# Performance work log

Hardware: AMD Instinct MI355X
Metric: run time of the kernel (lower is better)

## Reference

```python
import jax, jax.numpy as jnp
import numpy as np

IB = 8      # input/hidden activation bits
ABMVM = 8   # gate activation bits after MVM
ABNM = 8    # near-memory compute bits
NL = 0.05   # analog noise level
CY_DIV = 2.0
CY_SCALE = 2.0


def quant_pass(x, wb, sign):
    # Faithful port of QuantFunc.forward: clip/clamp then fake-quant (round to grid).
    if wb is None or wb == 0:
        return x
    if sign:
        delta = 0.0 if wb == 1 else 1.0 / (2.0 ** (wb - 1))
        x = jnp.clip(x, -1.0 + delta, 1.0 - delta)
    else:
        x = jnp.clip(x, 0.0, 1.0)
    if wb == 1:
        return jnp.sign(x)
    scale = 2.0 ** (wb - 1) if sign else 2.0 ** wb
    return jnp.round(x * scale) / scale


def setup_inputs() -> dict:
    key = jax.random.key(0)
    ks = jax.random.split(key, 7)
    B, I, H = 4096, 1024, 1024
    return {
        "input": jax.random.normal(ks[0], (B, I), jnp.float32),
        "hx": jax.random.normal(ks[1], (B, H), jnp.float32),
        "cx": jax.random.normal(ks[2], (B, H), jnp.float32),
        "weight_ih": jax.random.normal(ks[3], (4 * H, I), jnp.float32) * 0.1,
        "weight_hh": jax.random.normal(ks[4], (4 * H, H), jnp.float32) * 0.1,
        "bias_ih": jax.random.normal(ks[5], (4 * H,), jnp.float32) * 0.1,
        "bias_hh": jax.random.normal(ks[6], (4 * H,), jnp.float32) * 0.1,
        "train": 0,
    }


def reference(input, hx, cx, weight_ih, weight_hh, bias_ih, bias_hh, train):
    # Per-call Gaussian noise (simulated analog hardware); fixed key for reproducibility.
    nk = jax.random.split(jax.random.key(42), 4)
    noise_w_ih = jax.random.normal(nk[0], weight_ih.T.shape, weight_ih.dtype) * weight_ih.max() * NL
    noise_w_hh = jax.random.normal(nk[1], weight_hh.T.shape, weight_hh.dtype) * weight_hh.max() * NL
    noise_b_ih = jax.random.normal(nk[2], bias_ih.shape, bias_ih.dtype) * bias_ih.max() * NL
    noise_b_hh = jax.random.normal(nk[3], bias_hh.shape, bias_hh.dtype) * bias_hh.max() * NL

    # gates: [B, 4H]
    gates = (quant_pass(input, IB, True) @ (weight_ih.T + noise_w_ih) + bias_ih + noise_b_ih
             + quant_pass(hx, IB, True) @ (weight_hh.T + noise_w_hh) + bias_hh + noise_b_hh)

    ingate, forgetgate, cellgate, outgate = jnp.split(gates, 4, axis=1)
    ingate = quant_pass(jax.nn.sigmoid(ingate), ABMVM, False)
    forgetgate = quant_pass(jax.nn.sigmoid(forgetgate), ABMVM, False)
    cellgate = quant_pass(jnp.tanh(cellgate), ABMVM, True)
    outgate = quant_pass(jax.nn.sigmoid(outgate), ABMVM, False)

    cy = quant_pass((quant_pass(forgetgate * cx, ABNM, True)
                     + quant_pass(ingate * cellgate, ABNM, True)) / CY_DIV, ABNM, True)
    hy = quant_pass(outgate * quant_pass(jnp.tanh(cy * CY_SCALE), ABNM, True), ABNM, True)
    return (hy, cy)
```

## Files before the change

### kernel.cpp

```cpp
#include <hip/hip_runtime.h>
#include <hip/hip_bf16.h>
#include <stdint.h>
#include <stddef.h>


#define PART 1

typedef __attribute__((ext_vector_type(8))) short bf16x8;
typedef __attribute__((ext_vector_type(4))) float f32x4;

#define BATCH 4096

#define WS_A_OFF    ((size_t)0)
#define WS_B_OFF    ((size_t)16 << 20)
#define WS_BIAS_OFF ((size_t)48 << 20)
#define WS_MAX_OFF  (WS_BIAS_OFF + 16384)

__host__ __device__ inline void tf2x32(uint32_t k0, uint32_t k1,
                                       uint32_t x0, uint32_t x1,
                                       uint32_t &o0, uint32_t &o1)
{
  const uint32_t k2 = k0 ^ k1 ^ 0x1BD11BDAu;
#define TFR(r) { x0 += x1; x1 = (x1 << (r)) | (x1 >> (32 - (r))); x1 ^= x0; }
  x0 += k0; x1 += k1;
  TFR(13) TFR(15) TFR(26) TFR(6)
  x0 += k1; x1 += k2 + 1u;
  TFR(17) TFR(29) TFR(16) TFR(24)
  x0 += k2; x1 += k0 + 2u;
  TFR(13) TFR(15) TFR(26) TFR(6)
  x0 += k0; x1 += k1 + 3u;
  TFR(17) TFR(29) TFR(16) TFR(24)
  x0 += k1; x1 += k2 + 4u;
  TFR(13) TFR(15) TFR(26) TFR(6)
  x0 += k2; x1 += k0 + 5u;
#undef TFR
  o0 = x0; o1 = x1;
}

__device__ inline uint32_t jax_bits32(uint32_t k0, uint32_t k1, uint32_t i, uint32_t size)
{
#if PART
  uint32_t a, b;
  tf2x32(k0, k1, 0u, i, a, b);
  return a ^ b;
#else
  uint32_t half = size >> 1, a, b;
  if (i < half) { tf2x32(k0, k1, i, i + half, a, b); return a; }
  tf2x32(k0, k1, i - half, i, a, b); return b;
#endif
}

__device__ inline float bits_to_normal(uint32_t bits)
{
  float f = __uint_as_float((bits >> 9) | 0x3F800000u) - 1.0f;
  const float lo = -0x1.fffffep-1f;
  float u = fmaxf(lo, f * 2.0f + lo);
  float w = -log1pf(-u * u);
  float p;
  if (w < 5.0f) {
    w -= 2.5f;
    p = 2.81022636e-08f;
    p = fmaf(p, w, 3.43273939e-07f);
    p = fmaf(p, w, -3.5233877e-06f);
    p = fmaf(p, w, -4.39150654e-06f);
    p = fmaf(p, w, 0.00021858087f);
    p = fmaf(p, w, -0.00125372503f);
    p = fmaf(p, w, -0.00417768164f);
    p = fmaf(p, w, 0.246640727f);
    p = fmaf(p, w, 1.50140941f);
  } else {
    w = sqrtf(w) - 3.0f;
    p = -0.000200214257f;
    p = fmaf(p, w, 0.000100950558f);
    p = fmaf(p, w, 0.00134934322f);
    p = fmaf(p, w, -0.00367342844f);
    p = fmaf(p, w, 0.00573950773f);
    p = fmaf(p, w, -0.0076224613f);
    p = fmaf(p, w, 0.00943887047f);
    p = fmaf(p, w, 1.00167406f);
    p = fmaf(p, w, 2.83297682f);
  }
  return 0x1.6a09e6p+0f * (p * u);
}

__device__ inline float quantS8(float x)
{
  x = fminf(fmaxf(x, -0.9921875f), 0.9921875f);
  return rintf(x * 128.0f) * 0.0078125f;
}
__device__ inline float quantU8(float x)
{
  x = fminf(fmaxf(x, 0.0f), 1.0f);
  return rintf(x * 256.0f) * 0.00390625f;
}

#define LOG2E 1.44269504088896340736f
__device__ inline float sigmoid_fast(float x)
{
  float e = __builtin_amdgcn_exp2f(x * -LOG2E);
  return __builtin_amdgcn_rcpf(1.0f + e);
}
__device__ inline float tanh_fast(float x)
{
  float a = fabsf(x);
  float e = __builtin_amdgcn_exp2f(a * (-2.0f * LOG2E));
  float t = (1.0f - e) * __builtin_amdgcn_rcpf(1.0f + e);
  return copysignf(t, x);
}

__device__ inline unsigned short f2bf(float x)
{
  uint32_t b = __float_as_uint(x);
  return (unsigned short)((b + 0x7FFFu + ((b >> 16) & 1u)) >> 16);
}
__device__ inline float bf2f(unsigned short u) { return __uint_as_float(((uint32_t)u) << 16); }

__device__ inline float dec_max(uint32_t u)
{
  uint32_t bits = (u & 0x80000000u) ? (u ^ 0x80000000u) : ~u;
  return __uint_as_float(bits);
}

__global__ void init_max(uint32_t* mx)
{
  if (threadIdx.x < 4) mx[threadIdx.x] = 0u;
}

__global__ void kmax_all(const float4* __restrict__ wih, const float4* __restrict__ whh,
                         const float4* __restrict__ bih, const float4* __restrict__ bhh,
                         uint32_t* __restrict__ mx)
{
  const int blk = blockIdx.x;
  const float4* src; int n4, bl, nb; uint32_t* out;
  if (blk < 1024)      { src = wih; n4 = 1048576; bl = blk;        nb = 1024; out = mx + 0; }
  else if (blk < 2048) { src = whh; n4 = 1048576; bl = blk - 1024; nb = 1024; out = mx + 1; }
  else if (blk < 2052) { src = bih; n4 = 1024;    bl = blk - 2048; nb = 4;    out = mx + 2; }
  else                 { src = bhh; n4 = 1024;    bl = blk - 2052; nb = 4;    out = mx + 3; }

  float m = -3.4e38f;
  for (int i = bl * 256 + threadIdx.x; i < n4; i += nb * 256) {
    float4 v = src[i];
    m = fmaxf(fmaxf(m, fmaxf(v.x, v.y)), fmaxf(v.z, v.w));
  }
  for (int off = 32; off; off >>= 1) m = fmaxf(m, __shfl_down(m, off, 64));
  __shared__ float sm[4];
  if ((threadIdx.x & 63) == 0) sm[threadIdx.x >> 6] = m;
  __syncthreads();
  if (threadIdx.x == 0) {
    float bm = fmaxf(fmaxf(sm[0], sm[1]), fmaxf(sm[2], sm[3]));
    uint32_t bits = __float_as_uint(bm);
    uint32_t enc = (bits & 0x80000000u) ? ~bits : (bits | 0x80000000u);
    atomicMax(out, enc);
  }
}

__global__ void build_all(const float* __restrict__ wih, const float* __restrict__ whh,
                          const float4* __restrict__ in, const float4* __restrict__ hxp,
                          const float* __restrict__ bih, const float* __restrict__ bhh,
                          unsigned short* __restrict__ A, unsigned short* __restrict__ B,
                          float* __restrict__ biasE, const uint32_t* __restrict__ mxenc,
                          uint32_t kih0, uint32_t kih1, uint32_t khh0, uint32_t khh1,
                          uint32_t kbi0, uint32_t kbi1, uint32_t kbh0, uint32_t kbh1)
{
  const uint32_t blk = blockIdx.x;
  if (blk < 16384u) {
    uint32_t t = blk * 256u + threadIdx.x;
    uint32_t arr = t >> 21;
    uint32_t r = t & 2097151u;
    uint32_t kp = r & 511u;
    uint32_t n = r >> 9;
    const float* w = arr ? whh : wih;
    float mx = dec_max(mxenc[arr]);
    uint32_t key0 = arr ? khh0 : kih0, key1 = arr ? khh1 : kih1;
    uint32_t k0 = kp * 2u;
    uint32_t hiw = 0u, low = 0u;
#pragma unroll
    for (int e = 0; e < 2; ++e) {
      uint32_t k = k0 + (uint32_t)e;
      float nrm = bits_to_normal(jax_bits32(key0, key1, k * 4096u + n, 4194304u));
      float weff = w[(size_t)n * 1024u + k] + (nrm * mx) * 0.05f;
      unsigned short hi = f2bf(weff);
      unsigned short lob = f2bf(weff - bf2f(hi));
      hiw |= ((uint32_t)hi) << (16 * e);
      low |= ((uint32_t)lob) << (16 * e);
    }
    uint32_t np = (n & 1023u) * 4u + (n >> 10);
    size_t base = (size_t)np * 4096u + (arr ? 1024u : 0u) + k0;
    *reinterpret_cast<uint32_t*>(B + base) = hiw;
    *reinterpret_cast<uint32_t*>(B + base + 2048u) = low;
  } else if (blk < 24576u) {
    int t = (int)(blk - 16384u) * 256 + threadIdx.x;
    int b = t >> 9;
    int kq = t & 511;
    float4 v = (kq < 256) ? in[b * 256 + kq] : hxp[b * 256 + (kq - 256)];
    unsigned short o[4];
    o[0] = f2bf(quantS8(v.x)); o[1] = f2bf(quantS8(v.y));
    o[2] = f2bf(quantS8(v.z)); o[3] = f2bf(quantS8(v.w));
    *reinterpret_cast<uint64_t*>(A + (size_t)t * 4) = *reinterpret_cast<uint64_t*>(o);
  } else {
    uint32_t j = (blk - 24576u) * 256u + threadIdx.x;
    float mi = dec_max(mxenc[2]), mh = dec_max(mxenc[3]);
    float ni = (bits_to_normal(jax_bits32(kbi0, kbi1, j, 4096u)) * mi) * 0.05f;
    float nh = (bits_to_normal(jax_bits32(kbh0, kbh1, j, 4096u)) * mh) * 0.05f;
    biasE[(j & 1023u) * 4u + (j >> 10)] = ((bih[j] + ni) + bhh[j]) + nh;
  }
}

__device__ __forceinline__ void gload_lds16(const void* g, void* l)
{
  __builtin_amdgcn_global_load_lds((__attribute__((address_space(1))) void*)g,
                                   (__attribute__((address_space(3))) void*)l, 16, 0, 0);
}

#define VM0  asm volatile("s_waitcnt vmcnt(0)" ::: "memory")
#define NOVM
#define SBAR __builtin_amdgcn_s_barrier()
#define SCB  __builtin_amdgcn_sched_barrier(0)

#define BUFSZ 32768

#define STAGE_A(ts_, bi_)                                                         \
    { unsigned char* la_ = lds + (bi_) * BUFSZ; const int ka_ = (ts_) * 32;       \
      gload_lds16(Ar0 + ka_, la_ + tid * 16);                                     \
      gload_lds16(Ar1 + ka_, la_ + 4096 + tid * 16);                              \
      gload_lds16(Ar2 + ka_, la_ + 8192 + tid * 16);                              \
      gload_lds16(Ar3 + ka_, la_ + 12288 + tid * 16); }
#define STAGE_BH(ts_, bi_)                                                        \
    { unsigned char* la_ = lds + (bi_) * BUFSZ; const int ka_ = (ts_) * 32;       \
      gload_lds16(Br0 + ka_, la_ + 16384 + tid * 16);                             \
      gload_lds16(Br1 + ka_, la_ + 16384 + 4096 + tid * 16); }
#define STAGE_BL(ts_, bi_)                                                        \
    { unsigned char* la_ = lds + (bi_) * BUFSZ; const int ka_ = (ts_) * 32;       \
      gload_lds16(Br0 + 2048 + ka_, la_ + 24576 + tid * 16);                      \
      gload_lds16(Br1 + 2048 + ka_, la_ + 24576 + 4096 + tid * 16); }

#define TILE_ONE(t_, BUF_, BUFN_, DO_STAGE_, VM_ASM_)                             \
  {                                                                               \
    const unsigned char* pa_  = lds + (BUF_) * BUFSZ + aoff;                      \
    const unsigned char* pbh_ = lds + (BUF_) * BUFSZ + 16384 + boffU;             \
    const unsigned char* pbl_ = lds + (BUF_) * BUFSZ + 24576 + boffU;             \
    bf16x8 bh_[4], bl_[4], afL_[4], afH_[4];                                      \
    _Pragma("unroll") for (int n_ = 0; n_ < 4; ++n_)                              \
      bh_[n_] = *(const bf16x8*)(pbh_ + n_ * 1024);                               \
    _Pragma("unroll") for (int m_ = 0; m_ < 4; ++m_)                              \
      afL_[m_] = *(const bf16x8*)(pa_ + m_ * 1024);                               \
    if (DO_STAGE_) { STAGE_A((t_) + 1, BUFN_); }                                  \
    __builtin_amdgcn_s_setprio(1);                                                \
    _Pragma("unroll") for (int m_ = 0; m_ < 4; ++m_)                              \
      _Pragma("unroll") for (int n_ = 0; n_ < 4; ++n_)                            \
        acc[m_][n_] = __builtin_amdgcn_mfma_f32_16x16x32_bf16(afL_[m_], bh_[n_],  \
                                                              acc[m_][n_], 0, 0, 0); \
    __builtin_amdgcn_s_setprio(0);                                                \
    _Pragma("unroll") for (int m_ = 0; m_ < 4; ++m_)                              \
      afH_[m_] = *(const bf16x8*)(pa_ + (4 + m_) * 1024);                         \
    if (DO_STAGE_) { STAGE_BH((t_) + 1, BUFN_); }                                 \
    __builtin_amdgcn_s_setprio(1);                                                \
    _Pragma("unroll") for (int m_ = 0; m_ < 4; ++m_)                              \
      _Pragma("unroll") for (int n_ = 0; n_ < 4; ++n_)                            \
        acc[4 + m_][n_] = __builtin_amdgcn_mfma_f32_16x16x32_bf16(afH_[m_], bh_[n_], \
                                                              acc[4 + m_][n_], 0, 0, 0); \
    __builtin_amdgcn_s_setprio(0);                                                \
    _Pragma("unroll") for (int n_ = 0; n_ < 4; ++n_)                              \
      bl_[n_] = *(const bf16x8*)(pbl_ + n_ * 1024);                               \
    if (DO_STAGE_) { STAGE_BL((t_) + 1, BUFN_); }                                 \
    __builtin_amdgcn_s_setprio(1);                                                \
    _Pragma("unroll") for (int m_ = 0; m_ < 4; ++m_)                              \
      _Pragma("unroll") for (int n_ = 0; n_ < 4; ++n_)                            \
        acc[m_][n_] = __builtin_amdgcn_mfma_f32_16x16x32_bf16(afL_[m_], bl_[n_],  \
                                                              acc[m_][n_], 0, 0, 0); \
    _Pragma("unroll") for (int m_ = 0; m_ < 4; ++m_)                              \
      _Pragma("unroll") for (int n_ = 0; n_ < 4; ++n_)                            \
        acc[4 + m_][n_] = __builtin_amdgcn_mfma_f32_16x16x32_bf16(afH_[m_], bl_[n_], \
                                                              acc[4 + m_][n_], 0, 0, 0); \
    __builtin_amdgcn_s_setprio(0);                                                \
    VM_ASM_;                                                                      \
    SBAR; SCB;                                                                    \
  }

#define LTS 136

__global__ __launch_bounds__(256, 2) void gemm_gates(
    const unsigned short* __restrict__ A,
    const unsigned short* __restrict__ B,
    const float* __restrict__ bias,
    const float* __restrict__ cx,
    float* __restrict__ hy,
    float* __restrict__ cy)
{
  extern __shared__ unsigned char lds[];
  const int tid  = threadIdx.x;
  const int lane = tid & 63;
  const int wave = tid >> 6;
  const int wr = wave >> 1;
  const int wc = wave & 1;

  const int bid = blockIdx.x;
  const int wg  = (bid & 7) * 64 + (bid >> 3);
  const int brow = (wg & 15) * 256;
  const int bcol = (wg >> 4) * 128;

#define CHUNK_SRC(c_, sr_, sk_) \
    { int p_ = (c_) >> 3, lc_ = ((c_) & 7) ^ (p_ & 7); \
      sr_ = p_ * 2 + (lc_ >> 2); sk_ = (lc_ & 3) * 8; }
  int sr, sk;
  CHUNK_SRC(tid,        sr, sk);
  const unsigned short* Ar0 = A + (size_t)(brow + sr) * 2048 + sk;
  const unsigned short* Br0 = B + (size_t)(bcol + sr) * 4096 + sk;
  CHUNK_SRC(tid + 256,  sr, sk);
  const unsigned short* Ar1 = A + (size_t)(brow + sr) * 2048 + sk;
  const unsigned short* Br1 = B + (size_t)(bcol + sr) * 4096 + sk;
  CHUNK_SRC(tid + 512,  sr, sk);
  const unsigned short* Ar2 = A + (size_t)(brow + sr) * 2048 + sk;
  CHUNK_SRC(tid + 768,  sr, sk);
  const unsigned short* Ar3 = A + (size_t)(brow + sr) * 2048 + sk;
#undef CHUNK_SRC

  const int lrh = (lane & 15) >> 1;
  const int chk = ((((lane & 1) << 2) | (lane >> 4)) ^ lrh);
  const int aoff  = wr * 8192 + lrh * 128 + chk * 16;
  const int boffU = wc * 4096 + lrh * 128 + chk * 16;

  f32x4 acc[8][4] = {};

  STAGE_A(0, 0); STAGE_BH(0, 0); STAGE_BL(0, 0);
  VM0;
  SBAR; SCB;

#pragma unroll 1
  for (int t = 0; t < 63; ++t) {
    TILE_ONE(t, (t & 1), ((t + 1) & 1), 1, VM0);
  }
  TILE_ONE(63, 1, 0, 0, NOVM);

  float* LT = (float*)lds;
  const int col_local0 = wc * 64 + (lane & 15);
  const int lrow = (lane >> 4) << 2;
  const int h = tid & 31;
  const int hg = (bcol >> 2) + h;

#pragma unroll
  for (int hh = 0; hh < 2; ++hh) {
    __syncthreads();
#pragma unroll
    for (int m = 0; m < 4; ++m) {
#pragma unroll
      for (int n = 0; n < 4; ++n) {
        const int cl = col_local0 + n * 16;
        const float bv = bias[bcol + cl];
        const int lr0 = wr * 64 + m * 16 + lrow;
#pragma unroll
        for (int r = 0; r < 4; ++r)
          LT[(lr0 + r) * LTS + cl] = acc[hh * 4 + m][n][r] + bv;
      }
    }
    __syncthreads();
#pragma unroll
    for (int i = 0; i < 16; ++i) {
      const int lr = (tid >> 5) * 16 + i;
      const int grow = brow + ((lr >> 6) << 7) + hh * 64 + (lr & 63);
      const float4 q = *(const float4*)(LT + lr * LTS + 4 * h);
      const size_t oidx = (size_t)grow * 1024 + hg;
      float ing = quantU8(sigmoid_fast(q.x));
      float fg  = quantU8(sigmoid_fast(q.y));
      float cg  = quantS8(tanh_fast(q.z));
      float og  = quantU8(sigmoid_fast(q.w));
      float c0  = cx[oidx];
      float cyv = quantS8((quantS8(fg * c0) + quantS8(ing * cg)) * 0.5f);
      float hyv = quantS8(og * quantS8(tanh_fast(cyv * 2.0f)));
      hy[oidx] = hyv;
      cy[oidx] = cyv;
    }
  }
}

extern "C" void kernel_launch(void* const* d_in, const int* in_sizes, int n_in,
                              void* d_out, int out_size, void* d_ws, size_t ws_size,
                              hipStream_t stream)
{
  const float* input = (const float*)d_in[0];
  const float* hx    = (const float*)d_in[1];
  const float* cx    = (const float*)d_in[2];
  const float* wih   = (const float*)d_in[3];
  const float* whh   = (const float*)d_in[4];
  const float* bih   = (const float*)d_in[5];
  const float* bhh   = (const float*)d_in[6];
  (void)in_sizes; (void)n_in; (void)ws_size;

  uint8_t* ws = (uint8_t*)d_ws;
  unsigned short* A   = (unsigned short*)(ws + WS_A_OFF);
  unsigned short* B   = (unsigned short*)(ws + WS_B_OFF);
  float* biasE        = (float*)(ws + WS_BIAS_OFF);
  uint32_t* mx        = (uint32_t*)(ws + WS_MAX_OFF);

  uint32_t nk[4][2];
#if PART
  for (int i = 0; i < 4; ++i) tf2x32(0u, 42u, 0u, (uint32_t)i, nk[i][0], nk[i][1]);
#else
  {
    uint32_t w0[4], w1[4];
    for (int i = 0; i < 4; ++i) tf2x32(0u, 42u, (uint32_t)i, (uint32_t)(i + 4), w0[i], w1[i]);
    uint32_t out8[8] = {w0[0], w0[1], w0[2], w0[3], w1[0], w1[1], w1[2], w1[3]};
    for (int i = 0; i < 4; ++i) { nk[i][0] = out8[2 * i]; nk[i][1] = out8[2 * i + 1]; }
  }
#endif

  init_max<<<1, 64, 0, stream>>>(mx);
  kmax_all<<<2056, 256, 0, stream>>>((const float4*)wih, (const float4*)whh,
                                     (const float4*)bih, (const float4*)bhh, mx);
  build_all<<<24592, 256, 0, stream>>>(wih, whh, (const float4*)input, (const float4*)hx,
                                       bih, bhh, A, B, biasE, mx,
                                       nk[0][0], nk[0][1], nk[1][0], nk[1][1],
                                       nk[2][0], nk[2][1], nk[3][0], nk[3][1]);

  float* hy = (float*)d_out;
  float* cyp = hy + (size_t)BATCH * 1024;

  (void)hipFuncSetAttribute((const void*)gemm_gates,
                            hipFuncAttributeMaxDynamicSharedMemorySize, 71680);
  gemm_gates<<<dim3(512), dim3(256), 71680, stream>>>(A, B, biasE, cx, hy, cyp);
}
```

Baseline: 191.3 us.

## Enlarge GEMM tile to 256x256 with 8 waves and deeper K pipeline

The gates GEMM now uses 256x256 output tiles per workgroup with 512 threads (8 waves in a 2x4 layout) and 256 blocks, replacing 256x128 tiles with 4 waves. The K loop stages 64-wide tiles split into two 32-wide halves, issued two sub-stages ahead with partial vmcnt waits, and splits the MFMA work into phases separated by barriers. The goal is more operand reuse per byte loaded and better overlap of global-to-LDS loads with compute. The cost is much larger LDS use (139 KB), which may limit occupancy, plus more barriers per tile. The init_max kernel is also replaced with hipMemsetAsync.

Result: slower. 200.1 us (median of 4 runs) (+4.6%).

```diff
diff --git a/kernel.cpp b/kernel.cpp
--- a/kernel.cpp
+++ b/kernel.cpp
@@ -119,11 +119,6 @@
 {
   uint32_t bits = (u & 0x80000000u) ? (u ^ 0x80000000u) : ~u;
   return __uint_as_float(bits);
-}
-
-__global__ void init_max(uint32_t* mx)
-{
-  if (threadIdx.x < 4) mx[threadIdx.x] = 0u;
 }
 
 __global__ void kmax_all(const float4* __restrict__ wih, const float4* __restrict__ whh,
@@ -212,74 +207,62 @@
                                    (__attribute__((address_space(3))) void*)l, 16, 0, 0);
 }
 
+#define VM8  asm volatile("s_waitcnt vmcnt(8)" ::: "memory")
+#define VM4  asm volatile("s_waitcnt vmcnt(4)" ::: "memory")
 #define VM0  asm volatile("s_waitcnt vmcnt(0)" ::: "memory")
 #define NOVM
 #define SBAR __builtin_amdgcn_s_barrier()
 #define SCB  __builtin_amdgcn_sched_barrier(0)
-
-#define BUFSZ 32768
-
-#define STAGE_A(ts_, bi_)                                                         \
-    { unsigned char* la_ = lds + (bi_) * BUFSZ; const int ka_ = (ts_) * 32;       \
-      gload_lds16(Ar0 + ka_, la_ + tid * 16);                                     \
-      gload_lds16(Ar1 + ka_, la_ + 4096 + tid * 16);                              \
-      gload_lds16(Ar2 + ka_, la_ + 8192 + tid * 16);                              \
-      gload_lds16(Ar3 + ka_, la_ + 12288 + tid * 16); }
-#define STAGE_BH(ts_, bi_)                                                        \
-    { unsigned char* la_ = lds + (bi_) * BUFSZ; const int ka_ = (ts_) * 32;       \
-      gload_lds16(Br0 + ka_, la_ + 16384 + tid * 16);                             \
-      gload_lds16(Br1 + ka_, la_ + 16384 + 4096 + tid * 16); }
-#define STAGE_BL(ts_, bi_)                                                        \
-    { unsigned char* la_ = lds + (bi_) * BUFSZ; const int ka_ = (ts_) * 32;       \
-      gload_lds16(Br0 + 2048 + ka_, la_ + 24576 + tid * 16);                      \
-      gload_lds16(Br1 + 2048 + ka_, la_ + 24576 + 4096 + tid * 16); }
-
-#define TILE_ONE(t_, BUF_, BUFN_, DO_STAGE_, VM_ASM_)                             \
+#define LGKM0 asm volatile("s_waitcnt lgkmcnt(0)" ::: "memory")
+
+
+#define ST_A(ts_, ks_, bb_)                                                       \
+    { unsigned char* d_ = lds + (bb_) * 65536 + (ks_) * 16384;                    \
+      const int ka_ = (((ts_) * 64) + (ks_) * 32) & 2047;                         \
+      gload_lds16(Ap0 + ka_, d_ + tid * 16);                                      \
+      gload_lds16(Ap1 + ka_, d_ + 8192 + tid * 16); }
+#define ST_B(ts_, ks_, bb_)                                                       \
+    { unsigned char* d_ = lds + (bb_) * 65536 + 32768 + (ks_) * 16384;            \
+      const int kb_ = ((ts_) * 64) + (ks_) * 32;                                  \
+      gload_lds16(Bp0 + kb_, d_ + tid * 16);                                      \
+      gload_lds16(Bp1 + kb_, d_ + 8192 + tid * 16); }
+
+#define PHASE(bufb_, ks_, mh_, RDB_, STMT_, VMX_)                                 \
   {                                                                               \
-    const unsigned char* pa_  = lds + (BUF_) * BUFSZ + aoff;                      \
-    const unsigned char* pbh_ = lds + (BUF_) * BUFSZ + 16384 + boffU;             \
-    const unsigned char* pbl_ = lds + (BUF_) * BUFSZ + 24576 + boffU;             \
-    bf16x8 bh_[4], bl_[4], afL_[4], afH_[4];                                      \
-    _Pragma("unroll") for (int n_ = 0; n_ < 4; ++n_)                              \
-      bh_[n_] = *(const bf16x8*)(pbh_ + n_ * 1024);                               \
+    const unsigned char* ua_ = lds + (bufb_) + (ks_) * 16384;                     \
+    bf16x8 af_[4];                                                                \
+    if (RDB_) {                                                                   \
+      const unsigned char* vb_ = lds + (bufb_) + 32768 + (ks_) * 16384;           \
+      _Pragma("unroll") for (int n_ = 0; n_ < 4; ++n_)                            \
+        bfr[n_] = *(const bf16x8*)(vb_ + boff0 + n_ * 1024);                      \
+    }                                                                             \
     _Pragma("unroll") for (int m_ = 0; m_ < 4; ++m_)                              \
-      afL_[m_] = *(const bf16x8*)(pa_ + m_ * 1024);                               \
-    if (DO_STAGE_) { STAGE_A((t_) + 1, BUFN_); }                                  \
+      af_[m_] = *(const bf16x8*)(ua_ + aoff0 + ((mh_) * 4 + m_) * 1024);          \
+    STMT_;                                                                        \
+    SBAR;                                                                         \
+    LGKM0; SCB;                                                                   \
     __builtin_amdgcn_s_setprio(1);                                                \
     _Pragma("unroll") for (int m_ = 0; m_ < 4; ++m_)                              \
       _Pragma("unroll") for (int n_ = 0; n_ < 4; ++n_)                            \
-        acc[m_][n_] = __builtin_amdgcn_mfma_f32_16x16x32_bf16(afL_[m_], bh_[n_],  \
-                                                              acc[m_][n_], 0, 0, 0); \
+        acc[(mh_) * 4 + m_][n_] = __builtin_amdgcn_mfma_f32_16x16x32_bf16(        \
+            af_[m_], bfr[n_], acc[(mh_) * 4 + m_][n_], 0, 0, 0);                  \
     __builtin_amdgcn_s_setprio(0);                                                \
-    _Pragma("unroll") for (int m_ = 0; m_ < 4; ++m_)                              \
-      afH_[m_] = *(const bf16x8*)(pa_ + (4 + m_) * 1024);                         \
-    if (DO_STAGE_) { STAGE_BH((t_) + 1, BUFN_); }                                 \
-    __builtin_amdgcn_s_setprio(1);                                                \
-    _Pragma("unroll") for (int m_ = 0; m_ < 4; ++m_)                              \
-      _Pragma("unroll") for (int n_ = 0; n_ < 4; ++n_)                            \
-        acc[4 + m_][n_] = __builtin_amdgcn_mfma_f32_16x16x32_bf16(afH_[m_], bh_[n_], \
-                                                              acc[4 + m_][n_], 0, 0, 0); \
-    __builtin_amdgcn_s_setprio(0);                                                \
-    _Pragma("unroll") for (int n_ = 0; n_ < 4; ++n_)                              \
-      bl_[n_] = *(const bf16x8*)(pbl_ + n_ * 1024);                               \
-    if (DO_STAGE_) { STAGE_BL((t_) + 1, BUFN_); }                                 \
-    __builtin_amdgcn_s_setprio(1);                                                \
-    _Pragma("unroll") for (int m_ = 0; m_ < 4; ++m_)                              \
-      _Pragma("unroll") for (int n_ = 0; n_ < 4; ++n_)                            \
-        acc[m_][n_] = __builtin_amdgcn_mfma_f32_16x16x32_bf16(afL_[m_], bl_[n_],  \
-                                                              acc[m_][n_], 0, 0, 0); \
-    _Pragma("unroll") for (int m_ = 0; m_ < 4; ++m_)                              \
-      _Pragma("unroll") for (int n_ = 0; n_ < 4; ++n_)                            \
-        acc[4 + m_][n_] = __builtin_amdgcn_mfma_f32_16x16x32_bf16(afH_[m_], bl_[n_], \
-                                                              acc[4 + m_][n_], 0, 0, 0); \
-    __builtin_amdgcn_s_setprio(0);                                                \
-    VM_ASM_;                                                                      \
+    VMX_;                                                                         \
     SBAR; SCB;                                                                    \
   }
 
-#define LTS 136
-
-__global__ __launch_bounds__(256, 2) void gemm_gates(
+#define TILE(T_, ST01_, ST23_, VM1_, VM3_)                                        \
+  {                                                                               \
+    const int bufb_ = ((T_) & 1) * 65536;                                         \
+    PHASE(bufb_, 0, 0, 1, { if (ST01_) ST_A((T_) + 1, 1, ((T_) + 1) & 1); }, NOVM); \
+    PHASE(bufb_, 0, 1, 0, { if (ST01_) ST_B((T_) + 1, 1, ((T_) + 1) & 1); }, VM1_); \
+    PHASE(bufb_, 1, 0, 1, { if (ST23_) ST_A((T_) + 2, 0, (T_) & 1); }, NOVM);     \
+    PHASE(bufb_, 1, 1, 0, { if (ST23_) ST_B((T_) + 2, 0, (T_) & 1); }, VM3_);     \
+  }
+
+#define LTS 272
+
+__global__ __launch_bounds__(512, 2) void gemm_gates(
     const unsigned short* __restrict__ A,
     const unsigned short* __restrict__ B,
     const float* __restrict__ bias,
@@ -291,73 +274,75 @@
   const int tid  = threadIdx.x;
   const int lane = tid & 63;
   const int wave = tid >> 6;
-  const int wr = wave >> 1;
-  const int wc = wave & 1;
+  const int wr = wave >> 2;
+  const int wc = wave & 3;
 
   const int bid = blockIdx.x;
-  const int wg  = (bid & 7) * 64 + (bid >> 3);
+  const int wg  = (bid & 7) * 32 + (bid >> 3);
   const int brow = (wg & 15) * 256;
-  const int bcol = (wg >> 4) * 128;
+  const int bcol = (wg >> 4) * 256;
 
 #define CHUNK_SRC(c_, sr_, sk_) \
     { int p_ = (c_) >> 3, lc_ = ((c_) & 7) ^ (p_ & 7); \
       sr_ = p_ * 2 + (lc_ >> 2); sk_ = (lc_ & 3) * 8; }
   int sr, sk;
-  CHUNK_SRC(tid,        sr, sk);
-  const unsigned short* Ar0 = A + (size_t)(brow + sr) * 2048 + sk;
-  const unsigned short* Br0 = B + (size_t)(bcol + sr) * 4096 + sk;
-  CHUNK_SRC(tid + 256,  sr, sk);
-  const unsigned short* Ar1 = A + (size_t)(brow + sr) * 2048 + sk;
-  const unsigned short* Br1 = B + (size_t)(bcol + sr) * 4096 + sk;
-  CHUNK_SRC(tid + 512,  sr, sk);
-  const unsigned short* Ar2 = A + (size_t)(brow + sr) * 2048 + sk;
-  CHUNK_SRC(tid + 768,  sr, sk);
-  const unsigned short* Ar3 = A + (size_t)(brow + sr) * 2048 + sk;
+  CHUNK_SRC(tid,       sr, sk);
+  const unsigned short* Ap0 = A + (size_t)(brow + sr) * 2048 + sk;
+  const unsigned short* Bp0 = B + (size_t)(bcol + sr) * 4096 + sk;
+  CHUNK_SRC(tid + 512, sr, sk);
+  const unsigned short* Ap1 = A + (size_t)(brow + sr) * 2048 + sk;
+  const unsigned short* Bp1 = B + (size_t)(bcol + sr) * 4096 + sk;
 #undef CHUNK_SRC
 
   const int lrh = (lane & 15) >> 1;
   const int chk = ((((lane & 1) << 2) | (lane >> 4)) ^ lrh);
-  const int aoff  = wr * 8192 + lrh * 128 + chk * 16;
-  const int boffU = wc * 4096 + lrh * 128 + chk * 16;
+  const int aoff0 = wr * 8192 + lrh * 128 + chk * 16;
+  const int boff0 = wc * 4096 + lrh * 128 + chk * 16;
 
   f32x4 acc[8][4] = {};
-
-  STAGE_A(0, 0); STAGE_BH(0, 0); STAGE_BL(0, 0);
-  VM0;
+  bf16x8 bfr[4];
+
+  ST_A(0, 0, 0); ST_B(0, 0, 0);
+  ST_A(0, 1, 0); ST_B(0, 1, 0);
+  ST_A(1, 0, 1); ST_B(1, 0, 1);
+  VM8;
   SBAR; SCB;
 
 #pragma unroll 1
-  for (int t = 0; t < 63; ++t) {
-    TILE_ONE(t, (t & 1), ((t + 1) & 1), 1, VM0);
-  }
-  TILE_ONE(63, 1, 0, 0, NOVM);
+  for (int T = 0; T < 62; ++T) {
+    TILE(T, 1, 1, VM4, VM4);
+  }
+  TILE(62, 1, 0, VM4, VM4);
+  TILE(63, 0, 0, VM0, NOVM);
 
   float* LT = (float*)lds;
   const int col_local0 = wc * 64 + (lane & 15);
   const int lrow = (lane >> 4) << 2;
-  const int h = tid & 31;
+  const int h = tid & 63;
   const int hg = (bcol >> 2) + h;
 
 #pragma unroll
   for (int hh = 0; hh < 2; ++hh) {
     __syncthreads();
-#pragma unroll
-    for (int m = 0; m < 4; ++m) {
-#pragma unroll
-      for (int n = 0; n < 4; ++n) {
-        const int cl = col_local0 + n * 16;
-        const float bv = bias[bcol + cl];
-        const int lr0 = wr * 64 + m * 16 + lrow;
-#pragma unroll
-        for (int r = 0; r < 4; ++r)
-          LT[(lr0 + r) * LTS + cl] = acc[hh * 4 + m][n][r] + bv;
+    if (wr == hh) {
+#pragma unroll
+      for (int m = 0; m < 8; ++m) {
+#pragma unroll
+        for (int n = 0; n < 4; ++n) {
+          const int cl = col_local0 + n * 16;
+          const float bv = bias[bcol + cl];
+          const int lr0 = m * 16 + lrow;
+#pragma unroll
+          for (int r = 0; r < 4; ++r)
+            LT[(lr0 + r) * LTS + cl] = acc[m][n][r] + bv;
+        }
       }
     }
     __syncthreads();
 #pragma unroll
     for (int i = 0; i < 16; ++i) {
-      const int lr = (tid >> 5) * 16 + i;
-      const int grow = brow + ((lr >> 6) << 7) + hh * 64 + (lr & 63);
+      const int lr = (tid >> 6) * 16 + i;
+      const int grow = brow + hh * 128 + lr;
       const float4 q = *(const float4*)(LT + lr * LTS + 4 * h);
       const size_t oidx = (size_t)grow * 1024 + hg;
       float ing = quantU8(sigmoid_fast(q.x));
@@ -404,7 +389,7 @@
   }
 #endif
 
-  init_max<<<1, 64, 0, stream>>>(mx);
+  hipMemsetAsync(mx, 0, 16, stream);
   kmax_all<<<2056, 256, 0, stream>>>((const float4*)wih, (const float4*)whh,
                                      (const float4*)bih, (const float4*)bhh, mx);
   build_all<<<24592, 256, 0, stream>>>(wih, whh, (const float4*)input, (const float4*)hx,
@@ -416,6 +401,6 @@
   float* cyp = hy + (size_t)BATCH * 1024;
 
   (void)hipFuncSetAttribute((const void*)gemm_gates,
-                            hipFuncAttributeMaxDynamicSharedMemorySize, 71680);
-  gemm_gates<<<dim3(512), dim3(256), 71680, stream>>>(A, B, biasE, cx, hy, cyp);
-}
+                            hipFuncAttributeMaxDynamicSharedMemorySize, 139264);
+  gemm_gates<<<dim3(256), dim3(512), 139264, stream>>>(A, B, biasE, cx, hy, cyp);
+}
```
